# Kernel optimization log

Hardware: AMD Instinct MI355X
Metric: run time of the kernel (lower is better)

The kernel has to match this reference:

```python
import jax, jax.numpy as jnp
import numpy as np

K_SIZE = 5  # pred_k_size


def setup_inputs() -> dict:
    key = jax.random.key(0)
    k1, k2 = jax.random.split(key)
    bs, c, h, w = 4, 64, 160, 160
    fm = jax.random.normal(k1, (bs, c, h, w), dtype=jnp.float32)
    kernel = jax.random.normal(k2, (bs, K_SIZE * K_SIZE, h, w), dtype=jnp.float32)
    return {"fm": fm, "kernel": kernel, "dilation": 1}


def reference(fm, kernel, dilation):
    # fm: [bs, c, h, w]; kernel: [bs, k*k, h, w]
    bs, c, h, w = fm.shape
    k = K_SIZE
    pad = (k // 2) * dilation
    feat_padded = jnp.pad(fm, ((0, 0), (0, 0), (pad, pad), (pad, pad)))
    kern = jnp.flip(kernel, axis=1)  # torch.flip(kernel, dims=[1])
    # stack k*k shifted views: [bs, k*k, c, h, w]
    img_stack = jnp.stack(
        [
            feat_padded[:, :, i * dilation:i * dilation + h, j * dilation:j * dilation + w]
            for i in range(k)
            for j in range(k)
        ],
        axis=1,
    )
    # per-pixel weighted sum over the k*k taps -> [bs, c, h, w]
    res = jnp.sum(kern[:, :, None, :, :] * img_stack, axis=1)
    return res
```

## Files before the change

### kernel.cpp

```cpp
#include <hip/hip_runtime.h>

#define K   5
#define KK  25
#define H   160
#define W   160
#define C   64
#define BS  4
#define HW  (H * W)
#define CPG 4
#define BLK 256

__global__ __launch_bounds__(BLK, 6) void kconv_kernel(
    const float* __restrict__ fm,
    const float* __restrict__ kern,
    const int*  __restrict__ dil,
    float* __restrict__ out)
{
    const int q  = blockIdx.x * BLK + threadIdx.x;
    const int b  = blockIdx.z;
    const int cg = blockIdx.y;
    const int d  = dil[0];

    const int y = q / (W / 4);
    const int x = (q - y * (W / 4)) * 4;

    const float* fb = fm  + ((size_t)b * C + (size_t)cg * CPG) * HW;
    float*       ob = out + ((size_t)b * C + (size_t)cg * CPG) * HW + (size_t)y * W + x;
    const float* kb = kern + (size_t)b * KK * HW + (size_t)y * W + x;

    if (d == 1) {
        float acc[CPG][4];
#pragma unroll
        for (int c = 0; c < CPG; ++c)
#pragma unroll
            for (int p = 0; p < 4; ++p) acc[c][p] = 0.f;

        const int a_col = (x >= 2) ? (x - 2) : 0;
        const int d_col = (x + 4 <= W - 2) ? (x + 4) : (W - 2);

#pragma unroll
        for (int i = 0; i < K; ++i) {
            const int  yy  = y + i - 2;
            const bool rok = (yy >= 0) && (yy < H);
            const int  yr  = rok ? yy : 0;

            float wrow[K][4];
#pragma unroll
            for (int j = 0; j < K; ++j) {
                const int t = i * K + j;
                const float4 wv = *(const float4*)(kb + (size_t)(KK - 1 - t) * HW);
                const float wf[4] = {wv.x, wv.y, wv.z, wv.w};
#pragma unroll
                for (int p = 0; p < 4; ++p) {
                    const int col = x + p + j - 2;
                    const bool ok = rok && (col >= 0) && (col < W);
                    wrow[j][p] = ok ? wf[p] : 0.f;
                }
            }

            const float* rowbase = fb + (size_t)yr * W;
#pragma unroll
            for (int c = 0; c < CPG; ++c) {
                const float* r = rowbase + (size_t)c * HW;
                const float2 A  = *(const float2*)(r + a_col);
                const float2 Bv = *(const float2*)(r + x);
                const float2 Cv = *(const float2*)(r + x + 2);
                const float2 Dv = *(const float2*)(r + d_col);
                const float w8[8] = {A.x, A.y, Bv.x, Bv.y, Cv.x, Cv.y, Dv.x, Dv.y};
#pragma unroll
                for (int j = 0; j < K; ++j)
#pragma unroll
                    for (int p = 0; p < 4; ++p)
                        acc[c][p] = fmaf(wrow[j][p], w8[p + j], acc[c][p]);
            }
        }

#pragma unroll
        for (int c = 0; c < CPG; ++c) {
            const float4 o = {acc[c][0], acc[c][1], acc[c][2], acc[c][3]};
            *(float4*)(ob + (size_t)c * HW) = o;
        }
    } else {
#pragma unroll 1
        for (int p = 0; p < 4; ++p) {
            const int xx = x + p;
            float wgt[KK];
            int   offs[KK];
#pragma unroll 1
            for (int i = 0; i < K; ++i) {
                const int  yy  = y + (i - 2) * d;
                const bool yok = (yy >= 0) && (yy < H);
                const int  yc  = min(max(yy, 0), H - 1);
#pragma unroll 1
                for (int j = 0; j < K; ++j) {
                    const int  xc = xx + (j - 2) * d;
                    const bool ok = yok && (xc >= 0) && (xc < W);
                    const int  xcc = min(max(xc, 0), W - 1);
                    const int  t  = i * K + j;
                    wgt[t]  = ok ? kb[(size_t)(KK - 1 - t) * HW + p] : 0.f;
                    offs[t] = yc * W + xcc;
                }
            }
#pragma unroll 1
            for (int c = 0; c < CPG; ++c) {
                const float* fc = fb + (size_t)c * HW;
                float a2 = 0.f;
#pragma unroll 1
                for (int t = 0; t < KK; ++t) a2 = fmaf(wgt[t], fc[offs[t]], a2);
                ob[(size_t)c * HW + p] = a2;
            }
        }
    }
}

extern "C" void kernel_launch(void* const* d_in, const int* in_sizes, int n_in,
                              void* d_out, int out_size, void* d_ws, size_t ws_size,
                              hipStream_t stream)
{
    const float* fm   = (const float*)d_in[0];
    const float* kern = (const float*)d_in[1];
    const int*   dil  = (const int*)d_in[2];
    float*       out  = (float*)d_out;

    dim3 grid(HW / 4 / BLK, C / CPG, BS);
    kconv_kernel<<<grid, dim3(BLK), 0, stream>>>(fm, kern, dil, out);
}
```

Measured before the change: 109.7 us.

## Stage per-pixel kernel weights in LDS and share them across all channel groups

Each block now covers a 32x2 spatial tile for all 64 channels (16 channel groups of 4), instead of one channel group over a strip. The 25 tap weights for the tile are loaded once into shared memory and reused by every channel group. Before, each channel group re-read them from global memory. This adds a __syncthreads, a lower launch-bounds occupancy hint and smaller, narrower tiles, which may reduce coalescing of the feature-map row loads.

```diff
diff --git a/kernel.cpp b/kernel.cpp
--- a/kernel.cpp
+++ b/kernel.cpp
@@ -1,32 +1,55 @@
 #include <hip/hip_runtime.h>
 
-#define K   5
-#define KK  25
-#define H   160
-#define W   160
-#define C   64
-#define BS  4
-#define HW  (H * W)
-#define CPG 4
-#define BLK 256
+#define K    5
+#define KK   25
+#define H    160
+#define W    160
+#define C    64
+#define BS   4
+#define HW   (H * W)
+#define TX   32
+#define TY   2
+#define QX   (TX / 4)
+#define CPG  4
+#define NCG  (C / CPG)
+#define BLK  256
+#define WPAD 36
+#define WSL  (TY * WPAD)
 
-__global__ __launch_bounds__(BLK, 6) void kconv_kernel(
+__global__ __launch_bounds__(BLK, 5) void kconv_kernel(
     const float* __restrict__ fm,
     const float* __restrict__ kern,
     const int*  __restrict__ dil,
     float* __restrict__ out)
 {
-    const int q  = blockIdx.x * BLK + threadIdx.x;
-    const int b  = blockIdx.z;
-    const int cg = blockIdx.y;
+    __shared__ float wlds[KK][WSL];
+
+    const int tid = threadIdx.x;
+    const int b   = blockIdx.z;
+    const int x0  = blockIdx.x * TX;
+    const int y0  = blockIdx.y * TY;
+
+    const float* kbase = kern + (size_t)b * KK * HW;
+    for (int idx = tid; idx < KK * TY * QX; idx += BLK) {
+        const int tap = idx / (TY * QX);
+        const int rem = idx - tap * (TY * QX);
+        const int r   = rem / QX;
+        const int c4  = rem - r * QX;
+        const float4 v = *(const float4*)(kbase + (size_t)tap * HW +
+                                          (size_t)(y0 + r) * W + x0 + c4 * 4);
+        *(float4*)&wlds[KK - 1 - tap][r * WPAD + c4 * 4] = v;
+    }
+    __syncthreads();
+
+    const int qx = tid & (QX - 1);
+    const int ty = (tid >> 3) & (TY - 1);
+    const int cg = tid >> 4;
+    const int x  = x0 + qx * 4;
+    const int y  = y0 + ty;
     const int d  = dil[0];
-
-    const int y = q / (W / 4);
-    const int x = (q - y * (W / 4)) * 4;
 
     const float* fb = fm  + ((size_t)b * C + (size_t)cg * CPG) * HW;
     float*       ob = out + ((size_t)b * C + (size_t)cg * CPG) * HW + (size_t)y * W + x;
-    const float* kb = kern + (size_t)b * KK * HW + (size_t)y * W + x;
 
     if (d == 1) {
         float acc[CPG][4];
@@ -47,18 +70,17 @@
             float wrow[K][4];
 #pragma unroll
             for (int j = 0; j < K; ++j) {
-                const int t = i * K + j;
-                const float4 wv = *(const float4*)(kb + (size_t)(KK - 1 - t) * HW);
+                const float4 wv = *(const float4*)&wlds[i * K + j][ty * WPAD + qx * 4];
                 const float wf[4] = {wv.x, wv.y, wv.z, wv.w};
 #pragma unroll
                 for (int p = 0; p < 4; ++p) {
                     const int col = x + p + j - 2;
-                    const bool ok = rok && (col >= 0) && (col < W);
-                    wrow[j][p] = ok ? wf[p] : 0.f;
+                    wrow[j][p] = (rok && col >= 0 && col < W) ? wf[p] : 0.f;
                 }
             }
 
             const float* rowbase = fb + (size_t)yr * W;
+            float win[CPG][8];
 #pragma unroll
             for (int c = 0; c < CPG; ++c) {
                 const float* r = rowbase + (size_t)c * HW;
@@ -66,13 +88,19 @@
                 const float2 Bv = *(const float2*)(r + x);
                 const float2 Cv = *(const float2*)(r + x + 2);
                 const float2 Dv = *(const float2*)(r + d_col);
-                const float w8[8] = {A.x, A.y, Bv.x, Bv.y, Cv.x, Cv.y, Dv.x, Dv.y};
+                win[c][0] = A.x;  win[c][1] = A.y;
+                win[c][2] = Bv.x; win[c][3] = Bv.y;
+                win[c][4] = Cv.x; win[c][5] = Cv.y;
+                win[c][6] = Dv.x; win[c][7] = Dv.y;
+            }
+
+#pragma unroll
+            for (int c = 0; c < CPG; ++c)
 #pragma unroll
                 for (int j = 0; j < K; ++j)
 #pragma unroll
                     for (int p = 0; p < 4; ++p)
-                        acc[c][p] = fmaf(wrow[j][p], w8[p + j], acc[c][p]);
-            }
+                        acc[c][p] = fmaf(wrow[j][p], win[c][p + j], acc[c][p]);
         }
 
 #pragma unroll
@@ -81,9 +109,9 @@
             *(float4*)(ob + (size_t)c * HW) = o;
         }
     } else {
+        const float* kb = kern + (size_t)b * KK * HW + (size_t)y * W + x;
 #pragma unroll 1
         for (int p = 0; p < 4; ++p) {
-            const int xx = x + p;
             float wgt[KK];
             int   offs[KK];
 #pragma unroll 1
@@ -93,10 +121,10 @@
                 const int  yc  = min(max(yy, 0), H - 1);
 #pragma unroll 1
                 for (int j = 0; j < K; ++j) {
-                    const int  xc = xx + (j - 2) * d;
-                    const bool ok = yok && (xc >= 0) && (xc < W);
+                    const int  xc  = x + p + (j - 2) * d;
+                    const bool ok  = yok && (xc >= 0) && (xc < W);
                     const int  xcc = min(max(xc, 0), W - 1);
-                    const int  t  = i * K + j;
+                    const int  t   = i * K + j;
                     wgt[t]  = ok ? kb[(size_t)(KK - 1 - t) * HW + p] : 0.f;
                     offs[t] = yc * W + xcc;
                 }
@@ -122,6 +150,6 @@
     const int*   dil  = (const int*)d_in[2];
     float*       out  = (float*)d_out;
 
-    dim3 grid(HW / 4 / BLK, C / CPG, BS);
+    dim3 grid(W / TX, H / TY, BS);
     kconv_kernel<<<grid, dim3(BLK), 0, stream>>>(fm, kern, dil, out);
 }
```

Measured after the change: 270.6 us. 147% more time.
